# Performance work log

Hardware: AMD Instinct MI355X
Metric: run time of the kernel (lower is better)

The kernel has to match this reference:

```python
import jax, jax.numpy as jnp
import numpy as np

CH = 256
HEADS = 4
RED = 8  # SE reduction on 2*CH channels


def _conv2d(x, w, pad):
    # x: [b,c,h,w], w: [o,i,kh,kw]
    return jax.lax.conv_general_dilated(
        x, w, window_strides=(1, 1), padding=[(pad, pad), (pad, pad)],
        dimension_numbers=('NCHW', 'OIHW', 'NCHW'))


def setup_inputs() -> dict:
    key = jax.random.key(0)
    ks = jax.random.split(key, 12)
    b, c, h, w = 4, CH, 64, 64
    c2 = 2 * c
    s = 0.02
    inp = {
        'color_feat': jax.random.normal(ks[0], (b, c, h, w), jnp.float32),
        'gray_feat': jax.random.normal(ks[1], (b, c, h, w), jnp.float32),
        'Wq': jax.random.normal(ks[2], (c, c), jnp.float32) * s,
        'Wk': jax.random.normal(ks[3], (c, c), jnp.float32) * s,
        'Wv': jax.random.normal(ks[4], (c, c), jnp.float32) * s,
        'Wproj': jax.random.normal(ks[5], (c, c), jnp.float32) * s,
        'ca_w1': jax.random.normal(ks[6], (c2 // RED, c2), jnp.float32) * s,
        'ca_w2': jax.random.normal(ks[7], (c2, c2 // RED), jnp.float32) * s,
        'sa_w': jax.random.normal(ks[8], (1, 2, 7, 7), jnp.float32) * s,
        'fuse_w': jax.random.normal(ks[9], (c, c2, 3, 3), jnp.float32) * s,
        'bn_gamma': jnp.ones((c,), jnp.float32),
        'bn_beta': jnp.zeros((c,), jnp.float32),
        'bn_mean': jnp.zeros((c,), jnp.float32),
        'bn_var': jnp.ones((c,), jnp.float32),
    }
    return inp


def reference(color_feat, gray_feat, Wq, Wk, Wv, Wproj, ca_w1, ca_w2,
              sa_w, fuse_w, bn_gamma, bn_beta, bn_mean, bn_var):
    b, c, h, w = color_feat.shape
    nh = HEADS
    d = c // nh
    scale = d ** -0.5

    def heads(x, W):
        # 1x1 conv then split heads: [b,c,h,w] -> [b,nh,hw,d]
        y = jnp.einsum('bchw,oc->bohw', x, W)
        return y.reshape(b, nh, d, h * w).transpose(0, 1, 3, 2)

    q = heads(color_feat, Wq)
    k = heads(gray_feat, Wk)
    v = heads(gray_feat, Wv)

    attn = jax.nn.softmax(jnp.einsum('bnid,bnjd->bnij', q, k) * scale, axis=-1)
    out = jnp.einsum('bnij,bnjd->bnid', attn, v)
    out = out.transpose(0, 1, 3, 2).reshape(b, c, h, w)
    out = jnp.einsum('bchw,oc->bohw', out, Wproj)

    cat = jnp.concatenate([out, gray_feat], axis=1)  # [b,2c,h,w]

    # Channel attention (SE with shared MLP on avg- and max-pooled vectors)
    def mlp(z):
        return jax.nn.relu(z @ ca_w1.T) @ ca_w2.T
    avg = cat.mean(axis=(2, 3))
    mx = cat.max(axis=(2, 3))
    wch = jax.nn.sigmoid(mlp(avg) + mlp(mx))[:, :, None, None]
    cat = cat * wch

    # Spatial attention: channel-mean/max -> 7x7 conv -> sigmoid gate
    sa_in = jnp.stack([cat.mean(axis=1), cat.max(axis=1)], axis=1)  # [b,2,h,w]
    wsp = jax.nn.sigmoid(_conv2d(sa_in, sa_w, pad=3))
    cat = cat * wsp

    # Fuse: 3x3 conv -> BatchNorm (inference stats) -> LeakyReLU(0.2)
    y = _conv2d(cat, fuse_w, pad=1)
    inv = bn_gamma / jnp.sqrt(bn_var + 1e-5)
    y = (y - bn_mean[None, :, None, None]) * inv[None, :, None, None] + bn_beta[None, :, None, None]
    return jnp.where(y > 0, y, 0.2 * y)
```

## Files before the change

kernel.cpp:

```cpp
#include <hip/hip_runtime.h>
#include <hip/hip_bf16.h>
#include <stdint.h>

#define HW_ 4096

typedef short bf16x8 __attribute__((ext_vector_type(8)));
typedef short short4v __attribute__((ext_vector_type(4)));
typedef short short8v __attribute__((ext_vector_type(8)));
typedef float f32x4 __attribute__((ext_vector_type(4)));
typedef float f32x16 __attribute__((ext_vector_type(16)));
typedef uint32_t u32x4 __attribute__((ext_vector_type(4)));

__device__ inline unsigned short f2bf(float x) {
  uint32_t u = __builtin_bit_cast(uint32_t, x);
  uint32_t r = ((u >> 16) & 1u) + 0x7fffu;
  return (unsigned short)((u + r) >> 16);
}
__device__ inline uint32_t cvt_pk_bf16(float lo, float hi) {
  uint32_t r;
  asm("v_cvt_pk_bf16_f32 %0, %1, %2" : "=v"(r) : "v"(lo), "v"(hi));
  return r;
}
__device__ inline float bf_lo(uint32_t u) { return __builtin_bit_cast(float, u << 16); }
__device__ inline float bf_hi(uint32_t u) { return __builtin_bit_cast(float, u & 0xffff0000u); }
__device__ inline void gld_lds16(const unsigned short* g, unsigned short* l) {
  __builtin_amdgcn_global_load_lds((const __attribute__((address_space(1))) void*)g,
                                   (__attribute__((address_space(3))) void*)l, 16, 0, 0);
}

#define WAIT_BARRIER(VMSTR)                                                  \
  asm volatile("s_waitcnt " VMSTR "\n\ts_barrier" ::: "memory");             \
  __builtin_amdgcn_sched_barrier(0);

__global__ __launch_bounds__(256) void xconv_kernel(
    const float* __restrict__ X, unsigned short* __restrict__ Y) {
  const int i = blockIdx.x * 256 + threadIdx.x;
  const int p = i & 4095;
  const int cg = (i >> 12) & 31;
  const int b = i >> 17;
  const float* src = X + ((size_t)b * 256 + cg * 8) * HW_ + p;
  float v[8];
#pragma unroll
  for (int e = 0; e < 8; ++e) v[e] = src[(size_t)e * HW_];
  uint4 o;
  o.x = cvt_pk_bf16(v[0], v[1]);
  o.y = cvt_pk_bf16(v[2], v[3]);
  o.z = cvt_pk_bf16(v[4], v[5]);
  o.w = cvt_pk_bf16(v[6], v[7]);
  *(uint4*)&Y[((size_t)(b * 32 + cg) * HW_ + p) * 8] = o;
}

__global__ __launch_bounds__(256) void prep_kernel(
    const float* __restrict__ Wq, const float* __restrict__ Wk,
    const float* __restrict__ Wv, const float* __restrict__ Wp,
    const float* __restrict__ fw,
    unsigned short* __restrict__ WqB, unsigned short* __restrict__ WkB,
    unsigned short* __restrict__ WvB, unsigned short* __restrict__ WpB,
    unsigned short* __restrict__ wt) {
  const int blk = blockIdx.x;
  if (blk < 128) {
    const int which = blk >> 5;
    const float* W = which == 0 ? Wq : which == 1 ? Wk : which == 2 ? Wv : Wp;
    unsigned short* Y = which == 0 ? WqB : which == 1 ? WkB : which == 2 ? WvB : WpB;
    const int i = (blk & 31) * 256 + threadIdx.x;
    const int o = i & 255;
    const int cg = i >> 8;
    float4 a = *(const float4*)&W[(size_t)o * 256 + cg * 8];
    float4 bq = *(const float4*)&W[(size_t)o * 256 + cg * 8 + 4];
    uint4 ov;
    ov.x = cvt_pk_bf16(a.x, a.y);
    ov.y = cvt_pk_bf16(a.z, a.w);
    ov.z = cvt_pk_bf16(bq.x, bq.y);
    ov.w = cvt_pk_bf16(bq.z, bq.w);
    *(uint4*)&Y[((size_t)cg * 256 + o) * 8] = ov;
  } else {
    const size_t i = (size_t)(blk - 128) * 256 + threadIdx.x;
    const int oc = (int)(i >> 9);
    const int ic = (int)(i & 511);
    const float* src = fw + i * 9;
#pragma unroll
    for (int tap = 0; tap < 9; ++tap)
      wt[((size_t)tap * 256 + oc) * 512 + ic] = f2bf(src[tap]);
  }
}

#define GSTAGE(KS, BUF)                                                       \
  gld_lds16(Xb + ((size_t)((KS) * 2 + (t >> 7)) * HW_ + p0 + (t & 127)) * 8,  \
            &X_l[BUF][0][0][0] + (size_t)t * 8);
#define GCOMP(KS)                                                             \
  {                                                                           \
    bf16x8 af = *(const bf16x8*)&W_l[(KS) * 2 + g32][wo * 32 + n][0];         \
    bf16x8 b0 = *(const bf16x8*)&X_l[(KS) & 3][g32][wp * 64 + n][0];          \
    bf16x8 b1 = *(const bf16x8*)&X_l[(KS) & 3][g32][wp * 64 + 32 + n][0];     \
    acc[0] = __builtin_amdgcn_mfma_f32_32x32x16_bf16(af, b0, acc[0], 0, 0, 0);\
    acc[1] = __builtin_amdgcn_mfma_f32_32x32x16_bf16(af, b1, acc[1], 0, 0, 0);\
  }

__global__ __launch_bounds__(256) void gemm_mfma_kernel(
    const unsigned short* __restrict__ Xbf, const unsigned short* __restrict__ Wbf,
    void* __restrict__ Yv, int mode, float oscale) {
  __shared__ unsigned short W_l[32][64][8];
  __shared__ unsigned short X_l[4][2][128][8];
  const int t = threadIdx.x;
  const int w = t >> 6;
  const int l = t & 63;
  const int n = l & 31;
  const int g32 = l >> 5;
  const int p0 = blockIdx.x * 128;
  const int o0 = blockIdx.y * 64;
  const int b = blockIdx.z;
  const int wo = w >> 1, wp = w & 1;
  const unsigned short* Xb = Xbf + (size_t)b * 32 * HW_ * 8;

#pragma unroll
  for (int j = 0; j < 8; ++j) {
    const int i = j * 256 + t;
    gld_lds16(Wbf + ((size_t)(i >> 6) * 256 + o0 + (i & 63)) * 8,
              &W_l[0][0][0] + (size_t)i * 8);
  }
  GSTAGE(0, 0)
  GSTAGE(1, 1)
  GSTAGE(2, 2)

  f32x16 acc[2] = {};
  for (int ks = 0; ks < 13; ++ks) {
    WAIT_BARRIER("vmcnt(2)")
    GSTAGE(ks + 3, (ks + 3) & 3)
    GCOMP(ks)
  }
  WAIT_BARRIER("vmcnt(2)")
  GCOMP(13)
  WAIT_BARRIER("vmcnt(1)")
  GCOMP(14)
  WAIT_BARRIER("vmcnt(0)")
  GCOMP(15)

  if (mode == 1) {
    unsigned short* Y = (unsigned short*)Yv;
    const size_t bh = (size_t)b * 4 + blockIdx.y;
#pragma unroll
    for (int pf = 0; pf < 2; ++pf) {
      const int p = p0 + wp * 64 + pf * 32 + n;
      unsigned short* dst = Y + (bh * HW_ + p) * 64 + wo * 32 + 4 * g32;
#pragma unroll
      for (int q = 0; q < 4; ++q) {
        uint2 uu;
        uu.x = cvt_pk_bf16(acc[pf][q * 4 + 0] * oscale, acc[pf][q * 4 + 1] * oscale);
        uu.y = cvt_pk_bf16(acc[pf][q * 4 + 2] * oscale, acc[pf][q * 4 + 3] * oscale);
        *(uint2*)&dst[8 * q] = uu;
      }
    }
  } else {
    unsigned short* Y = (unsigned short*)Yv;
    const int cgb = (o0 + wo * 32) >> 3;
#pragma unroll
    for (int pf = 0; pf < 2; ++pf) {
      const int p = p0 + wp * 64 + pf * 32 + n;
#pragma unroll
      for (int q = 0; q < 4; ++q) {
        uint2 uu;
        uu.x = cvt_pk_bf16(acc[pf][q * 4 + 0], acc[pf][q * 4 + 1]);
        uu.y = cvt_pk_bf16(acc[pf][q * 4 + 2], acc[pf][q * 4 + 3]);
        *(uint2*)&Y[((size_t)(b * 32 + cgb + q) * HW_ + p) * 8 + 4 * g32] = uu;
      }
    }
  }
}

#define GCOMP_KV(KS)                                                          \
  {                                                                           \
    bf16x8 afk = *(const bf16x8*)&W_l[0][(KS) * 2 + g32][wo * 32 + n][0];     \
    bf16x8 afv = *(const bf16x8*)&W_l[1][(KS) * 2 + g32][wo * 32 + n][0];     \
    bf16x8 b0 = *(const bf16x8*)&X_l[(KS) & 3][g32][wp * 64 + n][0];          \
    bf16x8 b1 = *(const bf16x8*)&X_l[(KS) & 3][g32][wp * 64 + 32 + n][0];     \
    accK[0] = __builtin_amdgcn_mfma_f32_32x32x16_bf16(afk, b0, accK[0], 0, 0, 0); \
    accK[1] = __builtin_amdgcn_mfma_f32_32x32x16_bf16(afk, b1, accK[1], 0, 0, 0); \
    accV[0] = __builtin_amdgcn_mfma_f32_32x32x16_bf16(afv, b0, accV[0], 0, 0, 0); \
    accV[1] = __builtin_amdgcn_mfma_f32_32x32x16_bf16(afv, b1, accV[1], 0, 0, 0); \
  }

__global__ __launch_bounds__(256) void gemm_kv_kernel(
    const unsigned short* __restrict__ Xbf, const unsigned short* __restrict__ WkB,
    const unsigned short* __restrict__ WvB, unsigned short* __restrict__ Kout,
    unsigned short* __restrict__ Vout) {
  __shared__ unsigned short W_l[2][32][64][8];
  __shared__ unsigned short X_l[4][2][128][8];
  const int t = threadIdx.x;
  const int w = t >> 6;
  const int l = t & 63;
  const int n = l & 31;
  const int g32 = l >> 5;
  const int p0 = blockIdx.x * 128;
  const int o0 = blockIdx.y * 64;
  const int b = blockIdx.z;
  const int wo = w >> 1, wp = w & 1;
  const unsigned short* Xb = Xbf + (size_t)b * 32 * HW_ * 8;

#pragma unroll
  for (int j = 0; j < 16; ++j) {
    const int i = j * 256 + t;
    const int ii = i & 2047;
    const unsigned short* Wsrc = (i >> 11) ? WvB : WkB;
    gld_lds16(Wsrc + ((size_t)(ii >> 6) * 256 + o0 + (ii & 63)) * 8,
              &W_l[0][0][0][0] + (size_t)i * 8);
  }
  GSTAGE(0, 0)
  GSTAGE(1, 1)
  GSTAGE(2, 2)

  f32x16 accK[2] = {};
  f32x16 accV[2] = {};
  for (int ks = 0; ks < 13; ++ks) {
    WAIT_BARRIER("vmcnt(2)")
    GSTAGE(ks + 3, (ks + 3) & 3)
    GCOMP_KV(ks)
  }
  WAIT_BARRIER("vmcnt(2)")
  GCOMP_KV(13)
  WAIT_BARRIER("vmcnt(1)")
  GCOMP_KV(14)
  WAIT_BARRIER("vmcnt(0)")
  GCOMP_KV(15)

  const size_t bh = (size_t)b * 4 + blockIdx.y;
#pragma unroll
  for (int pf = 0; pf < 2; ++pf) {
    const int p = p0 + wp * 64 + pf * 32 + n;
    unsigned short* dst = Kout + (bh * HW_ + p) * 64 + wo * 32 + 4 * g32;
#pragma unroll
    for (int q = 0; q < 4; ++q) {
      uint2 uu;
      uu.x = cvt_pk_bf16(accK[pf][q * 4 + 0], accK[pf][q * 4 + 1]);
      uu.y = cvt_pk_bf16(accK[pf][q * 4 + 2], accK[pf][q * 4 + 3]);
      *(uint2*)&dst[8 * q] = uu;
    }
  }
#pragma unroll
  for (int pf = 0; pf < 2; ++pf) {
    const int p = p0 + wp * 64 + pf * 32 + n;
#pragma unroll
    for (int r = 0; r < 16; ++r) {
      const int m = (r & 3) + 8 * (r >> 2) + 4 * g32;
      Vout[((size_t)b * 256 + o0 + wo * 32 + m) * HW_ + p] = f2bf(accV[pf][r]);
    }
  }
}

#define ATTN_STAGE(SB)                                                       \
  {                                                                          \
    gld_lds16(gKp, kst + (SB) * 4096);                                       \
    gld_lds16(gKp + 8 * 64, kst + (SB) * 4096 + 512);                        \
    gld_lds16(gVp, vst + (SB) * 4096);                                       \
    gld_lds16(gVp + (size_t)8 * HW_, vst + (SB) * 4096 + 512);               \
    gKp += 4096;                                                             \
    gVp += 64;                                                               \
  }

#define ATTN_COMPUTE(BUF)                                                    \
  {                                                                          \
    f32x16 aS0 = zero16, aS1 = zero16;                                       \
    __builtin_amdgcn_s_setprio(1);                                           \
    _Pragma("unroll") for (int s = 0; s < 4; ++s) {                          \
      bf16x8 kf0 = *(const bf16x8*)&k_l[(BUF) * 4096 + rowKA + kox[s]];      \
      bf16x8 kf1 = *(const bf16x8*)&k_l[(BUF) * 4096 + rowKB + kox[s]];      \
      aS0 = __builtin_amdgcn_mfma_f32_32x32x16_bf16(kf0, qf[s], aS0, 0, 0, 0); \
      aS1 = __builtin_amdgcn_mfma_f32_32x32x16_bf16(kf1, qf[s], aS1, 0, 0, 0); \
    }                                                                        \
    __builtin_amdgcn_s_setprio(0);                                           \
    float ex0[16], ex1[16];                                                  \
    _Pragma("unroll") for (int r = 0; r < 16; ++r) {                         \
      ex0[r] = __builtin_amdgcn_exp2f(aS0[r]);                               \
      ex1[r] = __builtin_amdgcn_exp2f(aS1[r]);                               \
    }                                                                        \
    float rsp0 = 0.f, rsp1 = 0.f, rsp2 = 0.f, rsp3 = 0.f;                    \
    _Pragma("unroll") for (int r = 0; r < 16; r += 4) {                      \
      rsp0 += ex0[r + 0] + ex1[r + 0];                                       \
      rsp1 += ex0[r + 1] + ex1[r + 1];                                       \
      rsp2 += ex0[r + 2] + ex1[r + 2];                                       \
      rsp3 += ex0[r + 3] + ex1[r + 3];                                       \
    }                                                                        \
    l_r += (rsp0 + rsp1) + (rsp2 + rsp3);                                    \
    union { u32x4 u4; bf16x8 v8; } pA, pB, pC, pD;                           \
    pA.u4 = (u32x4){cvt_pk_bf16(ex0[0], ex0[1]), cvt_pk_bf16(ex0[2], ex0[3]),    \
                    cvt_pk_bf16(ex0[4], ex0[5]), cvt_pk_bf16(ex0[6], ex0[7])};   \
    pB.u4 = (u32x4){cvt_pk_bf16(ex0[8], ex0[9]), cvt_pk_bf16(ex0[10], ex0[11]),  \
                    cvt_pk_bf16(ex0[12], ex0[13]), cvt_pk_bf16(ex0[14], ex0[15])};\
    pC.u4 = (u32x4){cvt_pk_bf16(ex1[0], ex1[1]), cvt_pk_bf16(ex1[2], ex1[3]),    \
                    cvt_pk_bf16(ex1[4], ex1[5]), cvt_pk_bf16(ex1[6], ex1[7])};   \
    pD.u4 = (u32x4){cvt_pk_bf16(ex1[8], ex1[9]), cvt_pk_bf16(ex1[10], ex1[11]),  \
                    cvt_pk_bf16(ex1[12], ex1[13]), cvt_pk_bf16(ex1[14], ex1[15])};\
    __builtin_amdgcn_s_setprio(1);                                           \
    _Pragma("unroll") for (int dh = 0; dh < 2; ++dh) {                       \
      const int rw = (BUF) * 4096 + (dh * 32 + n) * 64;                      \
      union { short4v h2[2]; bf16x8 v8; } v0, v1, v2, v3;                    \
      v0.h2[0] = *(const short4v*)&v_l[rw + voA0];                           \
      v0.h2[1] = *(const short4v*)&v_l[rw + voA1];                           \
      v1.h2[0] = *(const short4v*)&v_l[rw + voB0];                           \
      v1.h2[1] = *(const short4v*)&v_l[rw + voB1];                           \
      v2.h2[0] = *(const short4v*)&v_l[rw + voC0];                           \
      v2.h2[1] = *(const short4v*)&v_l[rw + voC1];                           \
      v3.h2[0] = *(const short4v*)&v_l[rw + voD0];                           \
      v3.h2[1] = *(const short4v*)&v_l[rw + voD1];                           \
      f32x16 ac = accO[dh];                                                  \
      ac = __builtin_amdgcn_mfma_f32_32x32x16_bf16(v0.v8, pA.v8, ac, 0, 0, 0); \
      ac = __builtin_amdgcn_mfma_f32_32x32x16_bf16(v1.v8, pB.v8, ac, 0, 0, 0); \
      ac = __builtin_amdgcn_mfma_f32_32x32x16_bf16(v2.v8, pC.v8, ac, 0, 0, 0); \
      ac = __builtin_amdgcn_mfma_f32_32x32x16_bf16(v3.v8, pD.v8, ac, 0, 0, 0); \
      accO[dh] = ac;                                                         \
    }                                                                        \
    __builtin_amdgcn_s_setprio(0);                                           \
  }

#define ATTN_PHASE(B, SB, VMSTR, DOST)                                       \
  WAIT_BARRIER(VMSTR)                                                        \
  if (DOST) { ATTN_STAGE(SB) }                                               \
  ATTN_COMPUTE(B)

__global__ __launch_bounds__(256) void attn_mfma_kernel(
    const unsigned short* __restrict__ Qb, const unsigned short* __restrict__ Kb,
    const unsigned short* __restrict__ Vb, unsigned short* __restrict__ Abf) {
  __shared__ unsigned short k_l[4 * 4096];
  __shared__ unsigned short v_l[4 * 4096];
  const int t = threadIdx.x;
  const int w = t >> 6;
  const int l = t & 63;
  const int n = l & 31;
  const int h = l >> 5;
  const int bid = blockIdx.x;
  const int gidx = (bid & 7) * 64 + (bid >> 3);
  const int bn = gidx >> 5;
  const int q0 = (gidx & 31) * 128 + w * 32;

  bf16x8 qf[4];
#pragma unroll
  for (int s = 0; s < 4; ++s)
    qf[s] = *(const bf16x8*)&Qb[((size_t)bn * HW_ + q0 + n) * 64 + s * 16 + h * 8];

  const int n7 = n & 7;
  const int rowKA = n * 64;
  const int rowKB = (32 + n) * 64;
  int kox[4];
#pragma unroll
  for (int s = 0; s < 4; ++s) kox[s] = ((2 * s + h) ^ n7) * 8;
  const int h4 = 4 * h;
  const int voA0 = ((0 ^ n7) * 8) + h4, voA1 = ((1 ^ n7) * 8) + h4;
  const int voB0 = ((2 ^ n7) * 8) + h4, voB1 = ((3 ^ n7) * 8) + h4;
  const int voC0 = ((4 ^ n7) * 8) + h4, voC1 = ((5 ^ n7) * 8) + h4;
  const int voD0 = ((6 ^ n7) * 8) + h4, voD1 = ((7 ^ n7) * 8) + h4;

  const int srow = 16 * w + (l >> 3);
  const int schunk = (l & 7) ^ ((l >> 3) & 7);
  const unsigned short* gKp = Kb + ((size_t)bn * HW_ + srow) * 64 + schunk * 8;
  const unsigned short* gVp = Vb + ((size_t)bn * 64 + srow) * HW_ + schunk * 8;
  unsigned short* kst = k_l + w * 1024;
  unsigned short* vst = v_l + w * 1024;

  f32x16 accO[2] = {};
  float l_r = 0.f;
  const f32x16 zero16 = {};

  ATTN_STAGE(0)
  ATTN_STAGE(1)

  for (int t4 = 0; t4 < 15; ++t4) {
    ATTN_PHASE(0, 2, "vmcnt(4)", 1)
    ATTN_PHASE(1, 3, "vmcnt(4)", 1)
    ATTN_PHASE(2, 0, "vmcnt(4)", 1)
    ATTN_PHASE(3, 1, "vmcnt(4)", 1)
  }
  ATTN_PHASE(0, 2, "vmcnt(4)", 1)
  ATTN_PHASE(1, 3, "vmcnt(4)", 1)
  ATTN_PHASE(2, 0, "vmcnt(4)", 0)
  ATTN_PHASE(3, 0, "vmcnt(0)", 0)

  const int head = bn & 3;
  const int bb = bn >> 2;
  const float lsum = l_r + __shfl_xor(l_r, 32);
  const float inv = 1.0f / lsum;
  const int pcol = q0 + n;
#pragma unroll
  for (int dh = 0; dh < 2; ++dh)
#pragma unroll
    for (int k4 = 0; k4 < 4; ++k4) {
      uint2 uu;
      uu.x = cvt_pk_bf16(accO[dh][k4 * 4 + 0] * inv, accO[dh][k4 * 4 + 1] * inv);
      uu.y = cvt_pk_bf16(accO[dh][k4 * 4 + 2] * inv, accO[dh][k4 * 4 + 3] * inv);
      const int cg = head * 8 + dh * 4 + k4;
      *(uint2*)&Abf[((size_t)(bb * 32 + cg) * HW_ + pcol) * 8 + h4] = uu;
    }
}

__global__ __launch_bounds__(256) void pool_kernel(
    const unsigned short* __restrict__ Pbf, const unsigned short* __restrict__ Gbf,
    float* __restrict__ psum, float* __restrict__ pmaxH) {
  const int cg = blockIdx.x;
  const int b = blockIdx.y;
  const int half = blockIdx.z;
  const int t = threadIdx.x;
  const unsigned short* P = Pbf + ((size_t)(b * 32 + cg) * HW_ + half * 2048) * 8;
  const unsigned short* G = Gbf + ((size_t)(b * 32 + cg) * HW_ + half * 2048) * 8;
  float s[16], m[16];
#pragma unroll
  for (int i = 0; i < 16; ++i) { s[i] = 0.f; m[i] = -1e30f; }
  for (int p = t; p < 2048; p += 256) {
    uint4 a = *(const uint4*)&P[(size_t)p * 8];
    uint4 gg = *(const uint4*)&G[(size_t)p * 8];
    const uint32_t ua[4] = {a.x, a.y, a.z, a.w};
    const uint32_t ug[4] = {gg.x, gg.y, gg.z, gg.w};
#pragma unroll
    for (int q = 0; q < 4; ++q) {
      const float a0 = bf_lo(ua[q]), a1 = bf_hi(ua[q]);
      const float g0 = bf_lo(ug[q]), g1 = bf_hi(ug[q]);
      s[q * 2] += a0; s[q * 2 + 1] += a1;
      m[q * 2] = fmaxf(m[q * 2], a0); m[q * 2 + 1] = fmaxf(m[q * 2 + 1], a1);
      s[8 + q * 2] += g0; s[8 + q * 2 + 1] += g1;
      m[8 + q * 2] = fmaxf(m[8 + q * 2], g0); m[8 + q * 2 + 1] = fmaxf(m[8 + q * 2 + 1], g1);
    }
  }
#pragma unroll
  for (int i = 0; i < 16; ++i)
#pragma unroll
    for (int off = 1; off < 64; off <<= 1) {
      s[i] += __shfl_xor(s[i], off);
      m[i] = fmaxf(m[i], __shfl_xor(m[i], off));
    }
  __shared__ float red[4][32];
  const int wv = t >> 6;
  if ((t & 63) == 0) {
#pragma unroll
    for (int i = 0; i < 16; ++i) { red[wv][i] = s[i]; red[wv][16 + i] = m[i]; }
  }
  __syncthreads();
  if (t < 32) {
    const float v0 = red[0][t], v1 = red[1][t], v2 = red[2][t], v3 = red[3][t];
    if (t < 16) {
      const int ch = (t < 8) ? cg * 8 + t : 256 + cg * 8 + (t - 8);
      psum[half * 2048 + b * 512 + ch] = v0 + v1 + v2 + v3;
    } else {
      const int i = t - 16;
      const int ch = (i < 8) ? cg * 8 + i : 256 + cg * 8 + (i - 8);
      pmaxH[half * 2048 + b * 512 + ch] = fmaxf(fmaxf(v0, v1), fmaxf(v2, v3));
    }
  }
}

__global__ __launch_bounds__(256) void se_kernel(
    const float* __restrict__ psum, const float* __restrict__ pmaxH,
    const float* __restrict__ w1, const float* __restrict__ w2,
    float* __restrict__ wch) {
  const int b = blockIdx.x;
  const int t = threadIdx.x;
  __shared__ float za[512], zm[512], hs[64];
  za[t] = (psum[b * 512 + t] + psum[2048 + b * 512 + t]) * (1.f / 4096.f);
  za[256 + t] = (psum[b * 512 + 256 + t] + psum[2048 + b * 512 + 256 + t]) * (1.f / 4096.f);
  zm[t] = fmaxf(pmaxH[b * 512 + t], pmaxH[2048 + b * 512 + t]);
  zm[256 + t] = fmaxf(pmaxH[b * 512 + 256 + t], pmaxH[2048 + b * 512 + 256 + t]);
  __syncthreads();
  if (t < 64) {
    float ha = 0.f, hm = 0.f;
    for (int c = 0; c < 512; ++c) {
      const float w = w1[t * 512 + c];
      ha += w * za[c];
      hm += w * zm[c];
    }
    hs[t] = fmaxf(ha, 0.f) + fmaxf(hm, 0.f);
  }
  __syncthreads();
  for (int o = t; o < 512; o += 256) {
    float acc = 0.f;
#pragma unroll
    for (int hh = 0; hh < 64; ++hh) acc += hs[hh] * w2[o * 64 + hh];
    wch[b * 512 + o] = 1.f / (1.f + __expf(-acc));
  }
}

__global__ __launch_bounds__(256) void sa_reduce_kernel(
    const unsigned short* __restrict__ Pbf, const unsigned short* __restrict__ Gbf,
    const float* __restrict__ wch, float* __restrict__ sa_in) {
  const int b = blockIdx.y;
  const int t = threadIdx.x;
  const int px = t & 63;
  const int sl = t >> 6;
  const int p = blockIdx.x * 64 + px;
  __shared__ float wl[512];
  __shared__ float sred[4][64], mred[4][64];
  wl[t] = wch[b * 512 + t];
  wl[256 + t] = wch[b * 512 + 256 + t];
  __syncthreads();
  float s = 0.f, mx = -1e30f;
#pragma unroll 4
  for (int k = 0; k < 16; ++k) {
    const int chunk = sl * 16 + k;
    const unsigned short* src = (chunk < 32)
        ? &Pbf[((size_t)(b * 32 + chunk) * HW_ + p) * 8]
        : &Gbf[((size_t)(b * 32 + (chunk - 32)) * HW_ + p) * 8];
    uint4 a = *(const uint4*)src;
    const uint32_t u[4] = {a.x, a.y, a.z, a.w};
#pragma unroll
    for (int q = 0; q < 4; ++q) {
      const float v0 = bf_lo(u[q]) * wl[chunk * 8 + q * 2];
      const float v1 = bf_hi(u[q]) * wl[chunk * 8 + q * 2 + 1];
      s += v0 + v1;
      mx = fmaxf(mx, fmaxf(v0, v1));
    }
  }
  sred[sl][px] = s;
  mred[sl][px] = mx;
  __syncthreads();
  if (sl == 0) {
    const float S = sred[0][px] + sred[1][px] + sred[2][px] + sred[3][px];
    const float M = fmaxf(fmaxf(mred[0][px], mred[1][px]), fmaxf(mred[2][px], mred[3][px]));
    sa_in[((size_t)b * 2 + 0) * HW_ + p] = S * (1.f / 512.f);
    sa_in[((size_t)b * 2 + 1) * HW_ + p] = M;
  }
}

__global__ __launch_bounds__(256) void sa_conv_kernel(
    const float* __restrict__ sa_in, const float* __restrict__ sa_w,
    float* __restrict__ wsp) {
  const int b = blockIdx.y;
  const int t = threadIdx.x;
  __shared__ float pl[2][64][64];
  __shared__ float wl[98];
  for (int e = t; e < 8192; e += 256) ((float*)pl)[e] = sa_in[(size_t)b * 8192 + e];
  if (t < 98) wl[t] = sa_w[t];
  __syncthreads();
  const int pix = blockIdx.x * 256 + t;
  const int y = pix >> 6, x = pix & 63;
  float acc = 0.f;
#pragma unroll
  for (int ic = 0; ic < 2; ++ic)
#pragma unroll
    for (int ky = 0; ky < 7; ++ky) {
      const int yy = y + ky - 3;
      if (yy < 0 || yy > 63) continue;
#pragma unroll
      for (int kx = 0; kx < 7; ++kx) {
        const int xx = x + kx - 3;
        if (xx < 0 || xx > 63) continue;
        acc += pl[ic][yy][xx] * wl[ic * 49 + ky * 7 + kx];
      }
    }
  wsp[(size_t)b * HW_ + pix] = 1.f / (1.f + __expf(-acc));
}

__global__ __launch_bounds__(256) void gate_kernel(
    const unsigned short* __restrict__ Pbf, const unsigned short* __restrict__ Gbf,
    const float* __restrict__ wch, const float* __restrict__ wsp,
    unsigned short* __restrict__ catg) {
  const int yp = blockIdx.x;
  const int xh = blockIdx.y;
  const int b = blockIdx.z;
  const int t = threadIdx.x;
  unsigned short* rowp = catg + ((size_t)b * 66 + yp) * 80 * 512;
  if (yp == 0 || yp == 65) {
    short8v z = {};
    for (int m = t; m < 2560; m += 256)
      *(short8v*)&rowp[((size_t)xh * 40 * 512) + m * 8] = z;
    return;
  }
  const int y = yp - 1;
  __shared__ unsigned short tile[32][512];
  __shared__ float wchl[512];
  __shared__ float wspl[32];
  for (int e = t; e < 512; e += 256) wchl[e] = wch[b * 512 + e];
  if (t < 32) wspl[t] = wsp[(size_t)b * HW_ + y * 64 + xh * 32 + t];
  {
    short8v z = {};
    const int xbase = xh ? 72 : 0;
    for (int m = t; m < 512; m += 256)
      *(short8v*)&rowp[(size_t)(xbase + (m >> 6)) * 512 + (m & 63) * 8] = z;
  }
  __syncthreads();
  const int xl = t & 31;
  const int x = xh * 32 + xl;
  const int cs = t >> 5;
  const float wx = wspl[xl];
#pragma unroll
  for (int k = 0; k < 8; ++k) {
    const int chunk = cs * 8 + k;
    const unsigned short* src = (chunk < 32)
        ? &Pbf[((size_t)(b * 32 + chunk) * HW_ + y * 64 + x) * 8]
        : &Gbf[((size_t)(b * 32 + (chunk - 32)) * HW_ + y * 64 + x) * 8];
    uint4 a = *(const uint4*)src;
    const uint32_t u[4] = {a.x, a.y, a.z, a.w};
    uint32_t o[4];
#pragma unroll
    for (int q = 0; q < 4; ++q) {
      const float lo = bf_lo(u[q]) * wchl[chunk * 8 + q * 2] * wx;
      const float hi = bf_hi(u[q]) * wchl[chunk * 8 + q * 2 + 1] * wx;
      o[q] = cvt_pk_bf16(lo, hi);
    }
    uint4 ov = {o[0], o[1], o[2], o[3]};
    *(uint4*)&tile[xl][(chunk ^ (xl & 7)) * 8] = ov;
  }
  __syncthreads();
#pragma unroll
  for (int j = 0; j < 8; ++j) {
    const int idx = j * 256 + t;
    const int xi_l = idx >> 6;
    const int c8 = idx & 63;
    uint4 v = *(const uint4*)&tile[xi_l][(c8 ^ (xi_l & 7)) * 8];
    *(uint4*)&rowp[(size_t)(xh * 32 + xi_l + 8) * 512 + c8 * 8] = v;
  }
}

__global__ __launch_bounds__(256) void fuse_mfma_kernel(
    const unsigned short* __restrict__ catg, const unsigned short* __restrict__ wt,
    const float* __restrict__ bn_g, const float* __restrict__ bn_b,
    const float* __restrict__ bn_m, const float* __restrict__ bn_v,
    float* __restrict__ out) {
  __shared__ unsigned short X_l[2][6][2][80][8];
  __shared__ unsigned short W_l[2][9][2][32][8];
  __shared__ float invl[32], shl[32];
  const int t = threadIdx.x;
  const int w = t >> 6;
  const int l = t & 63;
  const int n = l & 31;
  const int g = l >> 5;
  const int i = blockIdx.x;
  const int xcd = i & 7, slot = i >> 3;
  const int ocB = slot & 7;
  const int yb = xcd + 8 * (slot >> 3);
  const int y0 = (yb & 15) * 4;
  const int o0 = ocB * 32;
  const int b = yb >> 4;

  if (t < 32) {
    const float iv = bn_g[o0 + t] * rsqrtf(bn_v[o0 + t] + 1e-5f);
    invl[t] = iv;
    shl[t] = bn_b[o0 + t] - bn_m[o0 + t] * iv;
  }

  const unsigned short* catb = catg + ((size_t)b * 66 + y0) * 80 * 512;

  auto stageX = [&](int bi, int ic0) {
    for (int wc = w; wc < 15; wc += 4) {
      const int m = wc * 64 + l;
      const int lr = m / 160;
      const int rem = m - lr * 160;
      const int half = rem / 80;
      const int xi = rem - half * 80;
      gld_lds16(catb + ((size_t)lr * 80 + xi) * 512 + ic0 + half * 8,
                &X_l[bi][0][0][0][0] + (size_t)wc * 512);
    }
  };
  auto stageW = [&](int bi, int ic0) {
    for (int wc = w; wc < 9; wc += 4) {
      const int m = wc * 64 + l;
      const int tap = m >> 6;
      const int rem = m & 63;
      const int half = rem >> 5;
      const int oc = rem & 31;
      gld_lds16(wt + ((size_t)tap * 256 + o0 + oc) * 512 + ic0 + half * 8,
                &W_l[bi][0][0][0][0] + (size_t)wc * 512);
    }
  };

  f32x16 acc[2] = {};

  stageX(0, 0);
  stageW(0, 0);
  int buf = 0;
  for (int ks = 0; ks < 32; ++ks) {
    asm volatile("s_waitcnt vmcnt(0)" ::: "memory");
    __syncthreads();
    if (ks < 31) {
      stageX(buf ^ 1, (ks + 1) * 16);
      stageW(buf ^ 1, (ks + 1) * 16);
    }
    __builtin_amdgcn_s_setprio(1);
#pragma unroll
    for (int ky = 0; ky < 3; ++ky) {
      const int lr = w + ky;
#pragma unroll
      for (int kx = 0; kx < 3; ++kx) {
        const int tap = ky * 3 + kx;
        bf16x8 a0 = *(const bf16x8*)&W_l[buf][tap][g][n][0];
        bf16x8 b0 = *(const bf16x8*)&X_l[buf][lr][g][n + kx + 7][0];
        bf16x8 b1 = *(const bf16x8*)&X_l[buf][lr][g][32 + n + kx + 7][0];
        acc[0] = __builtin_amdgcn_mfma_f32_32x32x16_bf16(a0, b0, acc[0], 0, 0, 0);
        acc[1] = __builtin_amdgcn_mfma_f32_32x32x16_bf16(a0, b1, acc[1], 0, 0, 0);
      }
    }
    __builtin_amdgcn_s_setprio(0);
    buf ^= 1;
  }

#pragma unroll
  for (int pf = 0; pf < 2; ++pf)
#pragma unroll
    for (int r = 0; r < 16; ++r) {
      const int row = (r & 3) + 8 * (r >> 2) + 4 * g;
      const float yv = acc[pf][r] * invl[row] + shl[row];
      const float ov = yv > 0.f ? yv : 0.2f * yv;
      out[((size_t)b * 256 + o0 + row) * HW_ + (size_t)(y0 + w) * 64 + pf * 32 + n] = ov;
    }
}

extern "C" void kernel_launch(void* const* d_in, const int* in_sizes, int n_in,
                              void* d_out, int out_size, void* d_ws, size_t ws_size,
                              hipStream_t stream) {
  const float* color  = (const float*)d_in[0];
  const float* gray   = (const float*)d_in[1];
  const float* Wq     = (const float*)d_in[2];
  const float* Wk     = (const float*)d_in[3];
  const float* Wv     = (const float*)d_in[4];
  const float* Wproj  = (const float*)d_in[5];
  const float* ca_w1  = (const float*)d_in[6];
  const float* ca_w2  = (const float*)d_in[7];
  const float* sa_w   = (const float*)d_in[8];
  const float* fuse_w = (const float*)d_in[9];
  const float* bn_g   = (const float*)d_in[10];
  const float* bn_b   = (const float*)d_in[11];
  const float* bn_m   = (const float*)d_in[12];
  const float* bn_v   = (const float*)d_in[13];
  float* out = (float*)d_out;

  char* ws = (char*)d_ws;
  unsigned short* Cbf = (unsigned short*)(ws);
  unsigned short* Gbf = (unsigned short*)(ws + (8u << 20));
  unsigned short* Qbf = (unsigned short*)(ws + (16u << 20));
  unsigned short* Kbf = (unsigned short*)(ws + (24u << 20));
  unsigned short* Vbf = (unsigned short*)(ws + (32u << 20));
  unsigned short* Abf = (unsigned short*)(ws);
  unsigned short* Pbf = (unsigned short*)(ws + (16u << 20));
  unsigned short* catg = (unsigned short*)(ws + (24u << 20));
  unsigned short* WqB = (unsigned short*)(ws + (45u << 20));
  unsigned short* WkB = WqB + 65536;
  unsigned short* WvB = WkB + 65536;
  unsigned short* WpB = WvB + 65536;
  unsigned short* Wt  = (unsigned short*)(ws + (45u << 20) + (1u << 19));
  float* psum  = (float*)(ws + (48u << 20));
  float* pmaxH = psum + 4096;
  float* wch   = pmaxH + 4096;
  float* sa_in = wch + 2048;
  float* wsp   = sa_in + 32768;
  (void)in_sizes; (void)n_in; (void)out_size; (void)ws_size;

  const float qscale = 0.125f * 1.44269504f;

  prep_kernel<<<dim3(640), 256, 0, stream>>>(Wq, Wk, Wv, Wproj, fuse_w,
                                             WqB, WkB, WvB, WpB, Wt);
  xconv_kernel<<<dim3(2048), 256, 0, stream>>>(color, Cbf);
  xconv_kernel<<<dim3(2048), 256, 0, stream>>>(gray, Gbf);

  dim3 g_gemm(32, 4, 4);
  gemm_mfma_kernel<<<g_gemm, 256, 0, stream>>>(Cbf, WqB, Qbf, 1, qscale);
  gemm_kv_kernel<<<g_gemm, 256, 0, stream>>>(Gbf, WkB, WvB, Kbf, Vbf);
  attn_mfma_kernel<<<dim3(512), 256, 0, stream>>>(Qbf, Kbf, Vbf, Abf);
  gemm_mfma_kernel<<<g_gemm, 256, 0, stream>>>(Abf, WpB, Pbf, 3, 1.0f);

  pool_kernel<<<dim3(32, 4, 2), 256, 0, stream>>>(Pbf, Gbf, psum, pmaxH);
  se_kernel<<<dim3(4), 256, 0, stream>>>(psum, pmaxH, ca_w1, ca_w2, wch);
  sa_reduce_kernel<<<dim3(64, 4), 256, 0, stream>>>(Pbf, Gbf, wch, sa_in);
  sa_conv_kernel<<<dim3(16, 4), 256, 0, stream>>>(sa_in, sa_w, wsp);
  gate_kernel<<<dim3(66, 2, 4), 256, 0, stream>>>(Pbf, Gbf, wch, wsp, catg);
  fuse_mfma_kernel<<<dim3(512), 256, 0, stream>>>(catg, Wt, bn_g, bn_b, bn_m, bn_v, out);
}
```

Baseline: 252.9 us.

## Merge input conversion into prep, widen attention blocks, triple-buffer fuse conv

Folds the two xconv launches into prep_kernel so one launch converts the color and gray activations and the weights. The attention kernel moves to 512-thread blocks covering 256 queries each, so each K/V tile is staged once per block and shared by more queries, with fewer loads per thread. The fuse conv switches from double buffering with a full vmcnt(0) wait to a three-stage pipeline with partial waits, overlapping loads with MFMA compute. The cost is more LDS and possible occupancy loss, and the clamped duplicate loads in the staging loops add some redundant traffic.

```diff
diff --git a/kernel.cpp b/kernel.cpp
--- a/kernel.cpp
+++ b/kernel.cpp
@@ -32,37 +32,40 @@
   asm volatile("s_waitcnt " VMSTR "\n\ts_barrier" ::: "memory");             \
   __builtin_amdgcn_sched_barrier(0);
 
-__global__ __launch_bounds__(256) void xconv_kernel(
-    const float* __restrict__ X, unsigned short* __restrict__ Y) {
-  const int i = blockIdx.x * 256 + threadIdx.x;
-  const int p = i & 4095;
-  const int cg = (i >> 12) & 31;
-  const int b = i >> 17;
-  const float* src = X + ((size_t)b * 256 + cg * 8) * HW_ + p;
-  float v[8];
-#pragma unroll
-  for (int e = 0; e < 8; ++e) v[e] = src[(size_t)e * HW_];
-  uint4 o;
-  o.x = cvt_pk_bf16(v[0], v[1]);
-  o.y = cvt_pk_bf16(v[2], v[3]);
-  o.z = cvt_pk_bf16(v[4], v[5]);
-  o.w = cvt_pk_bf16(v[6], v[7]);
-  *(uint4*)&Y[((size_t)(b * 32 + cg) * HW_ + p) * 8] = o;
-}
-
 __global__ __launch_bounds__(256) void prep_kernel(
+    const float* __restrict__ color, const float* __restrict__ gray,
     const float* __restrict__ Wq, const float* __restrict__ Wk,
     const float* __restrict__ Wv, const float* __restrict__ Wp,
     const float* __restrict__ fw,
+    unsigned short* __restrict__ Cbf, unsigned short* __restrict__ Gbf,
     unsigned short* __restrict__ WqB, unsigned short* __restrict__ WkB,
     unsigned short* __restrict__ WvB, unsigned short* __restrict__ WpB,
     unsigned short* __restrict__ wt) {
   const int blk = blockIdx.x;
-  if (blk < 128) {
-    const int which = blk >> 5;
+  const int t = threadIdx.x;
+  if (blk < 4096) {
+    const float* X = (blk < 2048) ? color : gray;
+    unsigned short* Y = (blk < 2048) ? Cbf : Gbf;
+    const int i = (blk & 2047) * 256 + t;
+    const int p = i & 4095;
+    const int cg = (i >> 12) & 31;
+    const int b = i >> 17;
+    const float* src = X + ((size_t)b * 256 + cg * 8) * HW_ + p;
+    float v[8];
+#pragma unroll
+    for (int e = 0; e < 8; ++e) v[e] = src[(size_t)e * HW_];
+    uint4 o;
+    o.x = cvt_pk_bf16(v[0], v[1]);
+    o.y = cvt_pk_bf16(v[2], v[3]);
+    o.z = cvt_pk_bf16(v[4], v[5]);
+    o.w = cvt_pk_bf16(v[6], v[7]);
+    *(uint4*)&Y[((size_t)(b * 32 + cg) * HW_ + p) * 8] = o;
+  } else if (blk < 4224) {
+    const int bb = blk - 4096;
+    const int which = bb >> 5;
     const float* W = which == 0 ? Wq : which == 1 ? Wk : which == 2 ? Wv : Wp;
     unsigned short* Y = which == 0 ? WqB : which == 1 ? WkB : which == 2 ? WvB : WpB;
-    const int i = (blk & 31) * 256 + threadIdx.x;
+    const int i = (bb & 31) * 256 + t;
     const int o = i & 255;
     const int cg = i >> 8;
     float4 a = *(const float4*)&W[(size_t)o * 256 + cg * 8];
@@ -74,7 +77,7 @@
     ov.w = cvt_pk_bf16(bq.z, bq.w);
     *(uint4*)&Y[((size_t)cg * 256 + o) * 8] = ov;
   } else {
-    const size_t i = (size_t)(blk - 128) * 256 + threadIdx.x;
+    const size_t i = (size_t)(blk - 4224) * 256 + t;
     const int oc = (int)(i >> 9);
     const int ic = (int)(i & 511);
     const float* src = fw + i * 9;
@@ -249,9 +252,7 @@
 #define ATTN_STAGE(SB)                                                       \
   {                                                                          \
     gld_lds16(gKp, kst + (SB) * 4096);                                       \
-    gld_lds16(gKp + 8 * 64, kst + (SB) * 4096 + 512);                        \
     gld_lds16(gVp, vst + (SB) * 4096);                                       \
-    gld_lds16(gVp + (size_t)8 * HW_, vst + (SB) * 4096 + 512);               \
     gKp += 4096;                                                             \
     gVp += 64;                                                               \
   }
@@ -316,7 +317,7 @@
   if (DOST) { ATTN_STAGE(SB) }                                               \
   ATTN_COMPUTE(B)
 
-__global__ __launch_bounds__(256) void attn_mfma_kernel(
+__global__ __launch_bounds__(512) void attn_mfma_kernel(
     const unsigned short* __restrict__ Qb, const unsigned short* __restrict__ Kb,
     const unsigned short* __restrict__ Vb, unsigned short* __restrict__ Abf) {
   __shared__ unsigned short k_l[4 * 4096];
@@ -327,9 +328,9 @@
   const int n = l & 31;
   const int h = l >> 5;
   const int bid = blockIdx.x;
-  const int gidx = (bid & 7) * 64 + (bid >> 3);
-  const int bn = gidx >> 5;
-  const int q0 = (gidx & 31) * 128 + w * 32;
+  const int gidx = (bid & 7) * 32 + (bid >> 3);
+  const int bn = gidx >> 4;
+  const int q0 = (gidx & 15) * 256 + w * 32;
 
   bf16x8 qf[4];
 #pragma unroll
@@ -348,12 +349,12 @@
   const int voC0 = ((4 ^ n7) * 8) + h4, voC1 = ((5 ^ n7) * 8) + h4;
   const int voD0 = ((6 ^ n7) * 8) + h4, voD1 = ((7 ^ n7) * 8) + h4;
 
-  const int srow = 16 * w + (l >> 3);
-  const int schunk = (l & 7) ^ ((l >> 3) & 7);
+  const int srow = t >> 3;
+  const int schunk = (t & 7) ^ (srow & 7);
   const unsigned short* gKp = Kb + ((size_t)bn * HW_ + srow) * 64 + schunk * 8;
   const unsigned short* gVp = Vb + ((size_t)bn * 64 + srow) * HW_ + schunk * 8;
-  unsigned short* kst = k_l + w * 1024;
-  unsigned short* vst = v_l + w * 1024;
+  unsigned short* kst = k_l + w * 512;
+  unsigned short* vst = v_l + w * 512;
 
   f32x16 accO[2] = {};
   float l_r = 0.f;
@@ -363,14 +364,14 @@
   ATTN_STAGE(1)
 
   for (int t4 = 0; t4 < 15; ++t4) {
-    ATTN_PHASE(0, 2, "vmcnt(4)", 1)
-    ATTN_PHASE(1, 3, "vmcnt(4)", 1)
-    ATTN_PHASE(2, 0, "vmcnt(4)", 1)
-    ATTN_PHASE(3, 1, "vmcnt(4)", 1)
-  }
-  ATTN_PHASE(0, 2, "vmcnt(4)", 1)
-  ATTN_PHASE(1, 3, "vmcnt(4)", 1)
-  ATTN_PHASE(2, 0, "vmcnt(4)", 0)
+    ATTN_PHASE(0, 2, "vmcnt(2)", 1)
+    ATTN_PHASE(1, 3, "vmcnt(2)", 1)
+    ATTN_PHASE(2, 0, "vmcnt(2)", 1)
+    ATTN_PHASE(3, 1, "vmcnt(2)", 1)
+  }
+  ATTN_PHASE(0, 2, "vmcnt(2)", 1)
+  ATTN_PHASE(1, 3, "vmcnt(2)", 1)
+  ATTN_PHASE(2, 0, "vmcnt(2)", 0)
   ATTN_PHASE(3, 0, "vmcnt(0)", 0)
 
   const int head = bn & 3;
@@ -610,8 +611,8 @@
     const float* __restrict__ bn_g, const float* __restrict__ bn_b,
     const float* __restrict__ bn_m, const float* __restrict__ bn_v,
     float* __restrict__ out) {
-  __shared__ unsigned short X_l[2][6][2][80][8];
-  __shared__ unsigned short W_l[2][9][2][32][8];
+  __shared__ unsigned short X_l[3][6][2][80][8];
+  __shared__ unsigned short W_l[3][9][2][32][8];
   __shared__ float invl[32], shl[32];
   const int t = threadIdx.x;
   const int w = t >> 6;
@@ -634,58 +635,65 @@
 
   const unsigned short* catb = catg + ((size_t)b * 66 + y0) * 80 * 512;
 
-  auto stageX = [&](int bi, int ic0) {
-    for (int wc = w; wc < 15; wc += 4) {
-      const int m = wc * 64 + l;
+  auto stage = [&](int bi, int ic0) {
+    for (int wc = w; wc < 16; wc += 4) {
+      const int wcc = wc > 14 ? 14 : wc;
+      const int m = wcc * 64 + l;
       const int lr = m / 160;
       const int rem = m - lr * 160;
       const int half = rem / 80;
       const int xi = rem - half * 80;
       gld_lds16(catb + ((size_t)lr * 80 + xi) * 512 + ic0 + half * 8,
-                &X_l[bi][0][0][0][0] + (size_t)wc * 512);
-    }
-  };
-  auto stageW = [&](int bi, int ic0) {
-    for (int wc = w; wc < 9; wc += 4) {
-      const int m = wc * 64 + l;
+                &X_l[bi][0][0][0][0] + (size_t)wcc * 512);
+    }
+    for (int wc = w; wc < 12; wc += 4) {
+      const int wcc = wc > 8 ? 8 : wc;
+      const int m = wcc * 64 + l;
       const int tap = m >> 6;
       const int rem = m & 63;
       const int half = rem >> 5;
       const int oc = rem & 31;
       gld_lds16(wt + ((size_t)tap * 256 + o0 + oc) * 512 + ic0 + half * 8,
-                &W_l[bi][0][0][0][0] + (size_t)wc * 512);
+                &W_l[bi][0][0][0][0] + (size_t)wcc * 512);
     }
   };
 
+#define FUSE_COMP(BI)                                                        \
+  {                                                                          \
+    __builtin_amdgcn_s_setprio(1);                                           \
+    _Pragma("unroll") for (int ky = 0; ky < 3; ++ky) {                       \
+      const int lr = w + ky;                                                 \
+      _Pragma("unroll") for (int kx = 0; kx < 3; ++kx) {                     \
+        const int tap = ky * 3 + kx;                                         \
+        bf16x8 a0 = *(const bf16x8*)&W_l[BI][tap][g][n][0];                  \
+        bf16x8 b0 = *(const bf16x8*)&X_l[BI][lr][g][n + kx + 7][0];          \
+        bf16x8 b1 = *(const bf16x8*)&X_l[BI][lr][g][32 + n + kx + 7][0];     \
+        acc[0] = __builtin_amdgcn_mfma_f32_32x32x16_bf16(a0, b0, acc[0], 0, 0, 0); \
+        acc[1] = __builtin_amdgcn_mfma_f32_32x32x16_bf16(a0, b1, acc[1], 0, 0, 0); \
+      }                                                                      \
+    }                                                                        \
+    __builtin_amdgcn_s_setprio(0);                                           \
+  }
+
   f32x16 acc[2] = {};
-
-  stageX(0, 0);
-  stageW(0, 0);
-  int buf = 0;
-  for (int ks = 0; ks < 32; ++ks) {
-    asm volatile("s_waitcnt vmcnt(0)" ::: "memory");
-    __syncthreads();
-    if (ks < 31) {
-      stageX(buf ^ 1, (ks + 1) * 16);
-      stageW(buf ^ 1, (ks + 1) * 16);
-    }
-    __builtin_amdgcn_s_setprio(1);
-#pragma unroll
-    for (int ky = 0; ky < 3; ++ky) {
-      const int lr = w + ky;
-#pragma unroll
-      for (int kx = 0; kx < 3; ++kx) {
-        const int tap = ky * 3 + kx;
-        bf16x8 a0 = *(const bf16x8*)&W_l[buf][tap][g][n][0];
-        bf16x8 b0 = *(const bf16x8*)&X_l[buf][lr][g][n + kx + 7][0];
-        bf16x8 b1 = *(const bf16x8*)&X_l[buf][lr][g][32 + n + kx + 7][0];
-        acc[0] = __builtin_amdgcn_mfma_f32_32x32x16_bf16(a0, b0, acc[0], 0, 0, 0);
-        acc[1] = __builtin_amdgcn_mfma_f32_32x32x16_bf16(a0, b1, acc[1], 0, 0, 0);
-      }
-    }
-    __builtin_amdgcn_s_setprio(0);
-    buf ^= 1;
-  }
+  stage(0, 0);
+  stage(1, 16);
+  for (int kb = 0; kb < 10; ++kb) {
+    const int ks = kb * 3;
+    WAIT_BARRIER("vmcnt(7)")
+    stage(2, (ks + 2) * 16);
+    FUSE_COMP(0)
+    WAIT_BARRIER("vmcnt(7)")
+    stage(0, (ks + 3) * 16);
+    FUSE_COMP(1)
+    WAIT_BARRIER("vmcnt(7)")
+    stage(1, (ks + 4) * 16);
+    FUSE_COMP(2)
+  }
+  WAIT_BARRIER("vmcnt(7)")
+  FUSE_COMP(0)
+  WAIT_BARRIER("vmcnt(0)")
+  FUSE_COMP(1)
 
 #pragma unroll
   for (int pf = 0; pf < 2; ++pf)
@@ -740,15 +748,13 @@
 
   const float qscale = 0.125f * 1.44269504f;
 
-  prep_kernel<<<dim3(640), 256, 0, stream>>>(Wq, Wk, Wv, Wproj, fuse_w,
-                                             WqB, WkB, WvB, WpB, Wt);
-  xconv_kernel<<<dim3(2048), 256, 0, stream>>>(color, Cbf);
-  xconv_kernel<<<dim3(2048), 256, 0, stream>>>(gray, Gbf);
+  prep_kernel<<<dim3(4736), 256, 0, stream>>>(color, gray, Wq, Wk, Wv, Wproj, fuse_w,
+                                              Cbf, Gbf, WqB, WkB, WvB, WpB, Wt);
 
   dim3 g_gemm(32, 4, 4);
   gemm_mfma_kernel<<<g_gemm, 256, 0, stream>>>(Cbf, WqB, Qbf, 1, qscale);
   gemm_kv_kernel<<<g_gemm, 256, 0, stream>>>(Gbf, WkB, WvB, Kbf, Vbf);
-  attn_mfma_kernel<<<dim3(512), 256, 0, stream>>>(Qbf, Kbf, Vbf, Abf);
+  attn_mfma_kernel<<<dim3(256), 512, 0, stream>>>(Qbf, Kbf, Vbf, Abf);
   gemm_mfma_kernel<<<g_gemm, 256, 0, stream>>>(Abf, WpB, Pbf, 3, 1.0f);
 
   pool_kernel<<<dim3(32, 4, 2), 256, 0, stream>>>(Pbf, Gbf, psum, pmaxH);
```

Measured after the change: 242.9 us, median of 2. 4.0% less time.
